# Kernel optimization log

Hardware: AMD Instinct MI355X
Metric: run time of the kernel (lower is better)

The kernel has to match this reference:

```python
import jax, jax.numpy as jnp
import numpy as np

FEAT_DIM = 256
HEAD_DIM = 32
N_HEADS = FEAT_DIM // HEAD_DIM
SIZE = 8  # sqrt(max_seq_len)
P = SIZE * SIZE  # 64
B, G = 4, 1024


def _rel_pos_index(size: int) -> np.ndarray:
    coords = np.stack(np.meshgrid(np.arange(size), np.arange(size), indexing='ij'))
    flat = coords.reshape(2, -1)
    rel = flat[:, :, None] - flat[:, None, :]
    rel = rel.transpose(1, 2, 0).copy()
    rel[:, :, 0] += size - 1
    rel[:, :, 1] += size - 1
    rel[:, :, 0] *= 2 * size - 1
    return rel.sum(-1)  # [P, P], values in [0, (2*size-1)^2)


def setup_inputs() -> dict:
    key = jax.random.key(0)
    ks = jax.random.split(key, 6)
    d = FEAT_DIM
    w_std = d ** -0.5
    return {
        'x': jax.random.normal(ks[0], (B, G, P, d), dtype=jnp.float32),
        'Wqkv': jax.random.normal(ks[1], (d, 3 * d), dtype=jnp.float32) * w_std,
        'bqkv': jnp.zeros((3 * d,), dtype=jnp.float32),
        'Wm': jax.random.normal(ks[2], (d, d), dtype=jnp.float32) * w_std,
        'bm': jnp.zeros((d,), dtype=jnp.float32),
        'bias_table': jax.random.normal(ks[3], ((2 * SIZE - 1) ** 2, N_HEADS), dtype=jnp.float32) * 0.02,
        'rel_index': jnp.asarray(_rel_pos_index(SIZE), dtype=jnp.int32),
    }


def reference(x, Wqkv, bqkv, Wm, bm, bias_table, rel_index):
    Bb, Gg, Pp, D = x.shape
    H, DH = N_HEADS, HEAD_DIM
    scale = D ** -0.5  # note: scale uses feat_dim, as in the original
    qkv = x @ Wqkv + bqkv  # [B,G,P,3D]
    q, k, v = jnp.split(qkv, 3, axis=-1)
    q = q.reshape(Bb, Gg, Pp, H, DH)
    k = k.reshape(Bb, Gg, Pp, H, DH) * scale
    v = v.reshape(Bb, Gg, Pp, H, DH)
    scores = jnp.einsum('BGIHD,BGJHD->BGHIJ', q, k)  # [B,G,H,P,P]
    # gathered relative-position bias: [P,P,H] -> [1,1,H,P,P]
    bias = bias_table[rel_index]  # [P,P,H]
    bias = jnp.transpose(bias, (2, 0, 1))[None, None]  # [1,1,H,P,P]
    attn = jax.nn.softmax(scores + bias, axis=-1)
    out = jnp.einsum('BGHIJ,BGJHD->BGIHD', attn, v)
    out = out.reshape(Bb, Gg, Pp, D)
    return out @ Wm + bm
```

## Files before the change

### kernel.cpp

```cpp
#include <hip/hip_runtime.h>

typedef short short8 __attribute__((ext_vector_type(8)));
typedef float f32x4 __attribute__((ext_vector_type(4)));

#define D_FEAT 256
#define P_TOK  64

#define XB_OFF 0
#define SCR_OFF 16896
#define LDS_TOT 37376
#define STX 264
#define ST40 40
#define ST72 72

static __device__ __forceinline__ unsigned short f2b(float f) {
  union { float f; unsigned u; } v; v.f = f;
  unsigned r = v.u + 0x7FFFu + ((v.u >> 16) & 1u);
  return (unsigned short)(r >> 16);
}

__global__ void prep_w_kernel(const float* __restrict__ W, unsigned short* __restrict__ Wf,
                              int ncols, int total, int qkv) {
  const int tid = blockIdx.x * blockDim.x + threadIdx.x;
  if (tid >= total) return;
  const int l  = tid & 63;
  const int ks = (tid >> 6) & 7;
  const int nt = tid >> 9;
  int col;
  if (qkv) {
    const int wv = nt / 6, tt = nt % 6;
    col = (tt >> 1) * 256 + wv * 32 + (tt & 1) * 16 + (l & 15);
  } else {
    col = nt * 16 + (l & 15);
  }
  const int k0 = ks * 32 + (l >> 4) * 8;
  short8 v;
#pragma unroll
  for (int j = 0; j < 8; ++j) v[j] = (short)f2b(W[(size_t)(k0 + j) * ncols + col]);
  *reinterpret_cast<short8*>(&Wf[(size_t)tid * 8]) = v;
}

__global__ void prep_bias_kernel(const float* __restrict__ bt, const int* __restrict__ ri,
                                 float* __restrict__ bc) {
  const int tid = blockIdx.x * blockDim.x + threadIdx.x;
  if (tid >= 8192) return;
  const int l  = tid & 63;
  const int t  = (tid >> 6) & 15;
  const int h  = tid >> 10;
  const int mt = t >> 2, nt = t & 3;
  f32x4 v;
#pragma unroll
  for (int i = 0; i < 4; ++i) {
    const int r = mt * 16 + (l >> 4) * 4 + i;
    const int c = nt * 16 + (l & 15);
    v[i] = bt[ri[r * 64 + c] * 8 + h];
  }
  *reinterpret_cast<f32x4*>(&bc[(size_t)tid * 4]) = v;
}

__global__ __launch_bounds__(512, 4)
void win_attn_kernel(const float* __restrict__ x,
                     const float* __restrict__ bqkv,
                     const float* __restrict__ bm,
                     const unsigned short* __restrict__ Wqkv_f,
                     const unsigned short* __restrict__ Wm_f,
                     const float* __restrict__ bias_c,
                     float* __restrict__ out)
{
  __shared__ unsigned short sm[LDS_TOT];
  const int tid = threadIdx.x;
  const int w   = tid >> 6;
  const int l   = tid & 63;
  const int lr  = l & 15;
  const int lg  = l >> 4;
  const long long win = blockIdx.x;
  const float* xw = x + win * (P_TOK * D_FEAT);
  const int SW = SCR_OFF + w * 2560;

#pragma unroll
  for (int it = 0; it < 8; ++it) {
    const int f = it * 2048 + tid * 4;
    const int row = f >> 8, col = f & 255;
    const float4 v = *reinterpret_cast<const float4*>(xw + f);
    ushort4 b;
    b.x = f2b(v.x); b.y = f2b(v.y); b.z = f2b(v.z); b.w = f2b(v.w);
    *reinterpret_cast<ushort4*>(&sm[XB_OFF + row * STX + col]) = b;
  }
  __syncthreads();

  short8 qf[4], kf[4], vf[2][2];
#pragma unroll
  for (int m = 0; m < 3; ++m) {
    f32x4 acc[4][2];
    {
      float bb0 = bqkv[m * 256 + w * 32 + lr];
      float bb1 = bqkv[m * 256 + w * 32 + 16 + lr];
#pragma unroll
      for (int mt = 0; mt < 4; ++mt) {
        acc[mt][0] = (f32x4){bb0, bb0, bb0, bb0};
        acc[mt][1] = (f32x4){bb1, bb1, bb1, bb1};
      }
    }
#pragma unroll
    for (int ks = 0; ks < 8; ++ks) {
      short8 a[4];
#pragma unroll
      for (int mt = 0; mt < 4; ++mt)
        a[mt] = *reinterpret_cast<const short8*>(
            &sm[XB_OFF + (lr + 16 * mt) * STX + lg * 8 + ks * 32]);
#pragma unroll
      for (int sub = 0; sub < 2; ++sub) {
        const short8 bf = *reinterpret_cast<const short8*>(
            &Wqkv_f[(size_t)(((w * 6 + m * 2 + sub) * 8 + ks) * 64 + l) * 8]);
#pragma unroll
        for (int mt = 0; mt < 4; ++mt)
          acc[mt][sub] = __builtin_amdgcn_mfma_f32_16x16x32_bf16(a[mt], bf, acc[mt][sub], 0, 0, 0);
      }
    }

    if (m == 2) {
#pragma unroll
      for (int sub = 0; sub < 2; ++sub)
#pragma unroll
        for (int mt = 0; mt < 4; ++mt) {
          ushort4 b;
          b.x = f2b(acc[mt][sub][0]); b.y = f2b(acc[mt][sub][1]);
          b.z = f2b(acc[mt][sub][2]); b.w = f2b(acc[mt][sub][3]);
          *reinterpret_cast<ushort4*>(&sm[SW + (sub * 16 + lr) * ST72 + 16 * mt + 4 * lg]) = b;
        }
#pragma unroll
      for (int nt = 0; nt < 2; ++nt)
#pragma unroll
        for (int kh = 0; kh < 2; ++kh)
          vf[nt][kh] = *reinterpret_cast<const short8*>(
              &sm[SW + (lr + 16 * nt) * ST72 + kh * 32 + lg * 8]);
    } else {
      const float sc = (m == 1) ? 0.0625f : 1.0f;
#pragma unroll
      for (int sub = 0; sub < 2; ++sub)
#pragma unroll
        for (int mt = 0; mt < 4; ++mt)
#pragma unroll
          for (int i = 0; i < 4; ++i)
            sm[SW + (16 * mt + 4 * lg + i) * ST40 + sub * 16 + lr] = f2b(acc[mt][sub][i] * sc);
#pragma unroll
      for (int mt = 0; mt < 4; ++mt) {
        const short8 fr = *reinterpret_cast<const short8*>(
            &sm[SW + (lr + 16 * mt) * ST40 + lg * 8]);
        if (m == 0) qf[mt] = fr; else kf[mt] = fr;
      }
    }
  }

  f32x4 s[4][4];
#pragma unroll
  for (int mt = 0; mt < 4; ++mt)
#pragma unroll
    for (int nt = 0; nt < 4; ++nt) {
      const f32x4 bb = *reinterpret_cast<const f32x4*>(
          &bias_c[(size_t)((w * 16 + mt * 4 + nt) * 64 + l) * 4]);
      s[mt][nt] = __builtin_amdgcn_mfma_f32_16x16x32_bf16(qf[mt], kf[nt], bb, 0, 0, 0);
    }
#pragma unroll
  for (int mt = 0; mt < 4; ++mt)
#pragma unroll
    for (int i = 0; i < 4; ++i) {
      float mx = fmaxf(fmaxf(s[mt][0][i], s[mt][1][i]), fmaxf(s[mt][2][i], s[mt][3][i]));
      mx = fmaxf(mx, __shfl_xor(mx, 1));
      mx = fmaxf(mx, __shfl_xor(mx, 2));
      mx = fmaxf(mx, __shfl_xor(mx, 4));
      mx = fmaxf(mx, __shfl_xor(mx, 8));
      float e0 = __expf(s[mt][0][i] - mx);
      float e1 = __expf(s[mt][1][i] - mx);
      float e2 = __expf(s[mt][2][i] - mx);
      float e3 = __expf(s[mt][3][i] - mx);
      float sum = e0 + e1 + e2 + e3;
      sum += __shfl_xor(sum, 1);
      sum += __shfl_xor(sum, 2);
      sum += __shfl_xor(sum, 4);
      sum += __shfl_xor(sum, 8);
      const float rinv = 1.0f / sum;
      s[mt][0][i] = e0 * rinv; s[mt][1][i] = e1 * rinv;
      s[mt][2][i] = e2 * rinv; s[mt][3][i] = e3 * rinv;
    }

  f32x4 o[4][2];
#pragma unroll
  for (int mt = 0; mt < 4; ++mt)
#pragma unroll
    for (int nt = 0; nt < 2; ++nt)
      o[mt][nt] = (f32x4){0.f, 0.f, 0.f, 0.f};
#pragma unroll
  for (int kh = 0; kh < 2; ++kh) {
#pragma unroll
    for (int ntl = 0; ntl < 2; ++ntl)
#pragma unroll
      for (int mt = 0; mt < 4; ++mt)
#pragma unroll
        for (int i = 0; i < 4; ++i)
          sm[SW + (16 * mt + 4 * lg + i) * ST40 + ntl * 16 + lr] = f2b(s[mt][2 * kh + ntl][i]);
#pragma unroll
    for (int mt = 0; mt < 4; ++mt) {
      const short8 pa = *reinterpret_cast<const short8*>(
          &sm[SW + (lr + 16 * mt) * ST40 + lg * 8]);
#pragma unroll
      for (int nt = 0; nt < 2; ++nt)
        o[mt][nt] = __builtin_amdgcn_mfma_f32_16x16x32_bf16(pa, vf[nt][kh], o[mt][nt], 0, 0, 0);
    }
  }

  __syncthreads();
#pragma unroll
  for (int mt = 0; mt < 4; ++mt)
#pragma unroll
    for (int nt = 0; nt < 2; ++nt)
#pragma unroll
      for (int i = 0; i < 4; ++i)
        sm[XB_OFF + (16 * mt + 4 * lg + i) * STX + w * 32 + nt * 16 + lr] = f2b(o[mt][nt][i]);
  __syncthreads();

  f32x4 po[4][2];
  {
    float bm0 = bm[w * 32 + lr];
    float bm1 = bm[w * 32 + 16 + lr];
#pragma unroll
    for (int mt = 0; mt < 4; ++mt) {
      po[mt][0] = (f32x4){bm0, bm0, bm0, bm0};
      po[mt][1] = (f32x4){bm1, bm1, bm1, bm1};
    }
  }
#pragma unroll
  for (int ks = 0; ks < 8; ++ks) {
    short8 a[4];
#pragma unroll
    for (int mt = 0; mt < 4; ++mt)
      a[mt] = *reinterpret_cast<const short8*>(
          &sm[XB_OFF + (lr + 16 * mt) * STX + lg * 8 + ks * 32]);
#pragma unroll
    for (int nt = 0; nt < 2; ++nt) {
      const short8 bf = *reinterpret_cast<const short8*>(
          &Wm_f[(size_t)(((w * 2 + nt) * 8 + ks) * 64 + l) * 8]);
#pragma unroll
      for (int mt = 0; mt < 4; ++mt)
        po[mt][nt] = __builtin_amdgcn_mfma_f32_16x16x32_bf16(a[mt], bf, po[mt][nt], 0, 0, 0);
    }
  }

  float* ow = out + win * (P_TOK * D_FEAT);
#pragma unroll
  for (int mt = 0; mt < 4; ++mt)
#pragma unroll
    for (int nt = 0; nt < 2; ++nt)
#pragma unroll
      for (int i = 0; i < 4; ++i)
        ow[(16 * mt + 4 * lg + i) * 256 + w * 32 + nt * 16 + lr] = po[mt][nt][i];
}

extern "C" void kernel_launch(void* const* d_in, const int* in_sizes, int n_in,
                              void* d_out, int out_size, void* d_ws, size_t ws_size,
                              hipStream_t stream) {
  const float* x    = (const float*)d_in[0];
  const float* Wqkv = (const float*)d_in[1];
  const float* bqkv = (const float*)d_in[2];
  const float* Wm   = (const float*)d_in[3];
  const float* bm   = (const float*)d_in[4];
  const float* bt   = (const float*)d_in[5];
  const int*   ri   = (const int*)d_in[6];

  unsigned short* Wqkv_f = (unsigned short*)d_ws;
  unsigned short* Wm_f   = (unsigned short*)((char*)d_ws + 393216);
  float*          bias_c = (float*)((char*)d_ws + 524288);

  prep_w_kernel<<<48, 512, 0, stream>>>(Wqkv, Wqkv_f, 768, 24576, 1);
  prep_w_kernel<<<16, 512, 0, stream>>>(Wm, Wm_f, 256, 8192, 0);
  prep_bias_kernel<<<16, 512, 0, stream>>>(bt, ri, bias_c);

  const int nwin = in_sizes[0] / (P_TOK * D_FEAT);
  win_attn_kernel<<<nwin, 512, 0, stream>>>(x, bqkv, bm, Wqkv_f, Wm_f, bias_c, (float*)d_out);
}
```

Before: 262.1 us.

## Transpose output projection for vectorized stores, fold scales, defer softmax normalization

Swaps the MFMA operand roles in the output projection so each lane holds four consecutive output columns, which allows 16-byte float4 global stores instead of scalar strided stores. The key scale is folded into the prepped weights and bias. Softmax normalization is deferred to after the PV product. Float-to-bf16 conversion uses packed hardware conversion intrinsics. Together these cut store transactions and ALU work per window, at the cost of slightly different rounding.

```diff
diff --git a/kernel.cpp b/kernel.cpp
--- a/kernel.cpp
+++ b/kernel.cpp
@@ -1,10 +1,8 @@
 #include <hip/hip_runtime.h>
+#include <hip/hip_bf16.h>
 
 typedef short short8 __attribute__((ext_vector_type(8)));
 typedef float f32x4 __attribute__((ext_vector_type(4)));
-
-#define D_FEAT 256
-#define P_TOK  64
 
 #define XB_OFF 0
 #define SCR_OFF 16896
@@ -17,6 +15,11 @@
   union { float f; unsigned u; } v; v.f = f;
   unsigned r = v.u + 0x7FFFu + ((v.u >> 16) & 1u);
   return (unsigned short)(r >> 16);
+}
+static __device__ __forceinline__ unsigned pk2(float a, float b) {
+  union { __hip_bfloat162 h; unsigned u; } v;
+  v.h = __float22bfloat162_rn(make_float2(a, b));
+  return v.u;
 }
 
 __global__ void prep_w_kernel(const float* __restrict__ W, unsigned short* __restrict__ Wf,
@@ -26,17 +29,18 @@
   const int l  = tid & 63;
   const int ks = (tid >> 6) & 7;
   const int nt = tid >> 9;
-  int col;
+  int col; float scl = 1.0f;
   if (qkv) {
     const int wv = nt / 6, tt = nt % 6;
     col = (tt >> 1) * 256 + wv * 32 + (tt & 1) * 16 + (l & 15);
+    if ((tt >> 1) == 1) scl = 0.0625f;
   } else {
     col = nt * 16 + (l & 15);
   }
   const int k0 = ks * 32 + (l >> 4) * 8;
   short8 v;
 #pragma unroll
-  for (int j = 0; j < 8; ++j) v[j] = (short)f2b(W[(size_t)(k0 + j) * ncols + col]);
+  for (int j = 0; j < 8; ++j) v[j] = (short)f2b(W[(size_t)(k0 + j) * ncols + col] * scl);
   *reinterpret_cast<short8*>(&Wf[(size_t)tid * 8]) = v;
 }
 
@@ -74,7 +78,7 @@
   const int lr  = l & 15;
   const int lg  = l >> 4;
   const long long win = blockIdx.x;
-  const float* xw = x + win * (P_TOK * D_FEAT);
+  const float* xw = x + win * 16384;
   const int SW = SCR_OFF + w * 2560;
 
 #pragma unroll
@@ -82,9 +86,8 @@
     const int f = it * 2048 + tid * 4;
     const int row = f >> 8, col = f & 255;
     const float4 v = *reinterpret_cast<const float4*>(xw + f);
-    ushort4 b;
-    b.x = f2b(v.x); b.y = f2b(v.y); b.z = f2b(v.z); b.w = f2b(v.w);
-    *reinterpret_cast<ushort4*>(&sm[XB_OFF + row * STX + col]) = b;
+    *reinterpret_cast<uint2*>(&sm[XB_OFF + row * STX + col]) =
+        make_uint2(pk2(v.x, v.y), pk2(v.z, v.w));
   }
   __syncthreads();
 
@@ -95,6 +98,7 @@
     {
       float bb0 = bqkv[m * 256 + w * 32 + lr];
       float bb1 = bqkv[m * 256 + w * 32 + 16 + lr];
+      if (m == 1) { bb0 *= 0.0625f; bb1 *= 0.0625f; }
 #pragma unroll
       for (int mt = 0; mt < 4; ++mt) {
         acc[mt][0] = (f32x4){bb0, bb0, bb0, bb0};
@@ -122,12 +126,10 @@
 #pragma unroll
       for (int sub = 0; sub < 2; ++sub)
 #pragma unroll
-        for (int mt = 0; mt < 4; ++mt) {
-          ushort4 b;
-          b.x = f2b(acc[mt][sub][0]); b.y = f2b(acc[mt][sub][1]);
-          b.z = f2b(acc[mt][sub][2]); b.w = f2b(acc[mt][sub][3]);
-          *reinterpret_cast<ushort4*>(&sm[SW + (sub * 16 + lr) * ST72 + 16 * mt + 4 * lg]) = b;
-        }
+        for (int mt = 0; mt < 4; ++mt)
+          *reinterpret_cast<uint2*>(&sm[SW + (sub * 16 + lr) * ST72 + 16 * mt + 4 * lg]) =
+              make_uint2(pk2(acc[mt][sub][0], acc[mt][sub][1]),
+                         pk2(acc[mt][sub][2], acc[mt][sub][3]));
 #pragma unroll
       for (int nt = 0; nt < 2; ++nt)
 #pragma unroll
@@ -135,14 +137,18 @@
           vf[nt][kh] = *reinterpret_cast<const short8*>(
               &sm[SW + (lr + 16 * nt) * ST72 + kh * 32 + lg * 8]);
     } else {
-      const float sc = (m == 1) ? 0.0625f : 1.0f;
 #pragma unroll
       for (int sub = 0; sub < 2; ++sub)
 #pragma unroll
-        for (int mt = 0; mt < 4; ++mt)
-#pragma unroll
-          for (int i = 0; i < 4; ++i)
-            sm[SW + (16 * mt + 4 * lg + i) * ST40 + sub * 16 + lr] = f2b(acc[mt][sub][i] * sc);
+        for (int mt = 0; mt < 4; ++mt) {
+          const unsigned p01 = pk2(acc[mt][sub][0], acc[mt][sub][1]);
+          const unsigned p23 = pk2(acc[mt][sub][2], acc[mt][sub][3]);
+          const int b = SW + (16 * mt + 4 * lg) * ST40 + sub * 16 + lr;
+          sm[b]            = (unsigned short)p01;
+          sm[b + ST40]     = (unsigned short)(p01 >> 16);
+          sm[b + 2 * ST40] = (unsigned short)p23;
+          sm[b + 3 * ST40] = (unsigned short)(p23 >> 16);
+        }
 #pragma unroll
       for (int mt = 0; mt < 4; ++mt) {
         const short8 fr = *reinterpret_cast<const short8*>(
@@ -161,6 +167,7 @@
           &bias_c[(size_t)((w * 16 + mt * 4 + nt) * 64 + l) * 4]);
       s[mt][nt] = __builtin_amdgcn_mfma_f32_16x16x32_bf16(qf[mt], kf[nt], bb, 0, 0, 0);
     }
+  float rinv[4][4];
 #pragma unroll
   for (int mt = 0; mt < 4; ++mt)
 #pragma unroll
@@ -170,35 +177,39 @@
       mx = fmaxf(mx, __shfl_xor(mx, 2));
       mx = fmaxf(mx, __shfl_xor(mx, 4));
       mx = fmaxf(mx, __shfl_xor(mx, 8));
-      float e0 = __expf(s[mt][0][i] - mx);
-      float e1 = __expf(s[mt][1][i] - mx);
-      float e2 = __expf(s[mt][2][i] - mx);
-      float e3 = __expf(s[mt][3][i] - mx);
+      const float e0 = __expf(s[mt][0][i] - mx);
+      const float e1 = __expf(s[mt][1][i] - mx);
+      const float e2 = __expf(s[mt][2][i] - mx);
+      const float e3 = __expf(s[mt][3][i] - mx);
       float sum = e0 + e1 + e2 + e3;
       sum += __shfl_xor(sum, 1);
       sum += __shfl_xor(sum, 2);
       sum += __shfl_xor(sum, 4);
       sum += __shfl_xor(sum, 8);
-      const float rinv = 1.0f / sum;
-      s[mt][0][i] = e0 * rinv; s[mt][1][i] = e1 * rinv;
-      s[mt][2][i] = e2 * rinv; s[mt][3][i] = e3 * rinv;
+      rinv[mt][i] = 1.0f / sum;
+      s[mt][0][i] = e0; s[mt][1][i] = e1; s[mt][2][i] = e2; s[mt][3][i] = e3;
     }
 
   f32x4 o[4][2];
 #pragma unroll
   for (int mt = 0; mt < 4; ++mt)
 #pragma unroll
-    for (int nt = 0; nt < 2; ++nt)
-      o[mt][nt] = (f32x4){0.f, 0.f, 0.f, 0.f};
+    for (int nt = 0; nt < 2; ++nt) o[mt][nt] = (f32x4){0.f, 0.f, 0.f, 0.f};
 #pragma unroll
   for (int kh = 0; kh < 2; ++kh) {
 #pragma unroll
     for (int ntl = 0; ntl < 2; ++ntl)
 #pragma unroll
-      for (int mt = 0; mt < 4; ++mt)
-#pragma unroll
-        for (int i = 0; i < 4; ++i)
-          sm[SW + (16 * mt + 4 * lg + i) * ST40 + ntl * 16 + lr] = f2b(s[mt][2 * kh + ntl][i]);
+      for (int mt = 0; mt < 4; ++mt) {
+        const int nt = 2 * kh + ntl;
+        const unsigned p01 = pk2(s[mt][nt][0], s[mt][nt][1]);
+        const unsigned p23 = pk2(s[mt][nt][2], s[mt][nt][3]);
+        const int b = SW + (16 * mt + 4 * lg) * ST40 + ntl * 16 + lr;
+        sm[b]            = (unsigned short)p01;
+        sm[b + ST40]     = (unsigned short)(p01 >> 16);
+        sm[b + 2 * ST40] = (unsigned short)p23;
+        sm[b + 3 * ST40] = (unsigned short)(p23 >> 16);
+      }
 #pragma unroll
     for (int mt = 0; mt < 4; ++mt) {
       const short8 pa = *reinterpret_cast<const short8*>(
@@ -213,47 +224,46 @@
 #pragma unroll
   for (int mt = 0; mt < 4; ++mt)
 #pragma unroll
-    for (int nt = 0; nt < 2; ++nt)
-#pragma unroll
-      for (int i = 0; i < 4; ++i)
-        sm[XB_OFF + (16 * mt + 4 * lg + i) * STX + w * 32 + nt * 16 + lr] = f2b(o[mt][nt][i]);
+    for (int nt = 0; nt < 2; ++nt) {
+      const unsigned p01 = pk2(o[mt][nt][0] * rinv[mt][0], o[mt][nt][1] * rinv[mt][1]);
+      const unsigned p23 = pk2(o[mt][nt][2] * rinv[mt][2], o[mt][nt][3] * rinv[mt][3]);
+      const int b = XB_OFF + (16 * mt + 4 * lg) * STX + w * 32 + nt * 16 + lr;
+      sm[b]           = (unsigned short)p01;
+      sm[b + STX]     = (unsigned short)(p01 >> 16);
+      sm[b + 2 * STX] = (unsigned short)p23;
+      sm[b + 3 * STX] = (unsigned short)(p23 >> 16);
+    }
   __syncthreads();
 
-  f32x4 po[4][2];
-  {
-    float bm0 = bm[w * 32 + lr];
-    float bm1 = bm[w * 32 + 16 + lr];
-#pragma unroll
-    for (int mt = 0; mt < 4; ++mt) {
-      po[mt][0] = (f32x4){bm0, bm0, bm0, bm0};
-      po[mt][1] = (f32x4){bm1, bm1, bm1, bm1};
-    }
+  f32x4 po[2][4];
+#pragma unroll
+  for (int mt = 0; mt < 2; ++mt) {
+    const f32x4 bi = *reinterpret_cast<const f32x4*>(&bm[w * 32 + mt * 16 + 4 * lg]);
+#pragma unroll
+    for (int nt = 0; nt < 4; ++nt) po[mt][nt] = bi;
   }
 #pragma unroll
   for (int ks = 0; ks < 8; ++ks) {
-    short8 a[4];
-#pragma unroll
-    for (int mt = 0; mt < 4; ++mt)
-      a[mt] = *reinterpret_cast<const short8*>(
-          &sm[XB_OFF + (lr + 16 * mt) * STX + lg * 8 + ks * 32]);
-#pragma unroll
-    for (int nt = 0; nt < 2; ++nt) {
-      const short8 bf = *reinterpret_cast<const short8*>(
-          &Wm_f[(size_t)(((w * 2 + nt) * 8 + ks) * 64 + l) * 8]);
-#pragma unroll
-      for (int mt = 0; mt < 4; ++mt)
-        po[mt][nt] = __builtin_amdgcn_mfma_f32_16x16x32_bf16(a[mt], bf, po[mt][nt], 0, 0, 0);
-    }
-  }
-
-  float* ow = out + win * (P_TOK * D_FEAT);
-#pragma unroll
-  for (int mt = 0; mt < 4; ++mt)
-#pragma unroll
-    for (int nt = 0; nt < 2; ++nt)
-#pragma unroll
-      for (int i = 0; i < 4; ++i)
-        ow[(16 * mt + 4 * lg + i) * 256 + w * 32 + nt * 16 + lr] = po[mt][nt][i];
+    short8 bx[4];
+#pragma unroll
+    for (int nt = 0; nt < 4; ++nt)
+      bx[nt] = *reinterpret_cast<const short8*>(
+          &sm[XB_OFF + (lr + 16 * nt) * STX + lg * 8 + ks * 32]);
+#pragma unroll
+    for (int mt = 0; mt < 2; ++mt) {
+      const short8 af = *reinterpret_cast<const short8*>(
+          &Wm_f[(size_t)(((w * 2 + mt) * 8 + ks) * 64 + l) * 8]);
+#pragma unroll
+      for (int nt = 0; nt < 4; ++nt)
+        po[mt][nt] = __builtin_amdgcn_mfma_f32_16x16x32_bf16(af, bx[nt], po[mt][nt], 0, 0, 0);
+    }
+  }
+  float* ow = out + win * 16384;
+#pragma unroll
+  for (int mt = 0; mt < 2; ++mt)
+#pragma unroll
+    for (int nt = 0; nt < 4; ++nt)
+      *reinterpret_cast<f32x4*>(&ow[(lr + 16 * nt) * 256 + w * 32 + mt * 16 + 4 * lg]) = po[mt][nt];
 }
 
 extern "C" void kernel_launch(void* const* d_in, const int* in_sizes, int n_in,
@@ -275,6 +285,6 @@
   prep_w_kernel<<<16, 512, 0, stream>>>(Wm, Wm_f, 256, 8192, 0);
   prep_bias_kernel<<<16, 512, 0, stream>>>(bt, ri, bias_c);
 
-  const int nwin = in_sizes[0] / (P_TOK * D_FEAT);
+  const int nwin = in_sizes[0] / 16384;
   win_attn_kernel<<<nwin, 512, 0, stream>>>(x, bqkv, bm, Wqkv_f, Wm_f, bias_c, (float*)d_out);
 }
```

Result: slower. 286.3 us (+9.2%).
